# Performance work log

Hardware: AMD Instinct MI355X
Metric: run time of the kernel (lower is better)

The kernel has to match this reference:

```python
import jax, jax.numpy as jnp
import numpy as np

B, S, D, H, FF = 4, 1024, 1024, 8, 4096
DK = D // H
EPS = 1e-5


def layernorm(x, g, b):
    m = jnp.mean(x, axis=-1, keepdims=True)
    v = jnp.mean(jnp.square(x - m), axis=-1, keepdims=True)
    return (x - m) * jax.lax.rsqrt(v + EPS) * g + b


def setup_inputs() -> dict:
    key = jax.random.key(0)
    ks = jax.random.split(key, 8)
    w = lambda k, shape: jax.random.normal(k, shape, jnp.float32) * 0.02
    return {
        "x": jax.random.normal(ks[0], (B, S, D), jnp.float32),
        "mask": jnp.ones((B, 1, 1, S), jnp.int32),  # unused in 'infer' mode, kept for fidelity
        "g1": jnp.ones((D,), jnp.float32), "b1": jnp.zeros((D,), jnp.float32),
        "Wq": w(ks[1], (D, D)), "bq": jnp.zeros((D,), jnp.float32),
        "Wk": w(ks[2], (D, D)), "bk": jnp.zeros((D,), jnp.float32),
        "Wv": w(ks[3], (D, H * D)), "bv": jnp.zeros((H * D,), jnp.float32),
        "g2": jnp.ones((D,), jnp.float32), "b2": jnp.zeros((D,), jnp.float32),
        "W1": w(ks[4], (D, FF)), "bw1": jnp.zeros((FF,), jnp.float32),
        "W2": w(ks[5], (FF, D)), "bw2": jnp.zeros((D,), jnp.float32),
    }


def reference(x, mask, g1, b1, Wq, bq, Wk, bk, Wv, bv, g2, b2, W1, bw1, W2, bw2):
    # --- MultiHeadedAttention (mode='infer'; mask is ignored by this path) ---
    xn = layernorm(x, g1, b1)                                   # [B,S,D]
    q = (xn @ Wq + bq).reshape(B, S, H, DK).transpose(0, 2, 1, 3)  # [B,H,S,DK]
    k = (xn @ Wk + bk).reshape(B, S, H, DK).transpose(0, 2, 1, 3)  # [B,H,S,DK]
    v = (xn @ Wv + bv).reshape(B, S, H, D).transpose(0, 2, 1, 3)   # [B,H,S,D]
    scores = jnp.einsum('bhqd,bhkd->bhqk', q, k) / jnp.sqrt(jnp.float32(DK))
    p = jax.nn.softmax(scores, axis=-1)                          # [B,H,S,S]
    ctx = jnp.einsum('bhqk,bhkd->bhqd', p, v)                    # [B,H,S,D]
    # Source does x.view(-1, B, dim, h).sum(heads).view(B, S, dim) on the
    # contiguous [B,H,S,D] tensor: a raw row-major reshape, reproduced exactly.
    attn_out = ctx.reshape(S, B, D, H).sum(axis=-1).reshape(B, S, D)
    # --- residual + SublayerConnection (pre-norm GELU FFN) ---
    x1 = x + attn_out
    xn2 = layernorm(x1, g2, b2)
    ffn = jax.nn.gelu(xn2 @ W1 + bw1, approximate=False) @ W2 + bw2
    return x1 + ffn
```

## Files before the change

### kernel.cpp

```cpp
#include <hip/hip_runtime.h>
#include <hip/hip_bf16.h>
#include <math.h>

typedef __attribute__((ext_vector_type(8))) short   short8;
typedef __attribute__((ext_vector_type(4))) short   short4v;
typedef __attribute__((ext_vector_type(8))) __bf16  bf16x8;
typedef __attribute__((ext_vector_type(4))) float   f32x4;

typedef const __attribute__((address_space(1))) void cgv_t;
typedef __attribute__((address_space(3))) void lv_t;

__device__ __forceinline__ float bs2f(short s) {
  unsigned int u = ((unsigned int)(unsigned short)s) << 16;
  return __builtin_bit_cast(float, u);
}
__device__ __forceinline__ short f2bs(float f) {
  __hip_bfloat16 h = __float2bfloat16(f);
  return __builtin_bit_cast(short, h);
}
__device__ __forceinline__ void glds16(const short* g, short* l) {
  __builtin_amdgcn_global_load_lds((cgv_t*)g, (lv_t*)l, 16, 0, 0);
}


__global__ __launch_bounds__(256) void transpose_k(const float* __restrict__ in,
                                                   short* __restrict__ out,
                                                   int R, int C) {
  __shared__ __align__(16) short T[64 * 72];
  const int r0 = blockIdx.y * 64, c0 = blockIdx.x * 64;
  const int t = threadIdx.x;
  {
    const int rr = t >> 4;
    const int cc = (t & 15) << 2;
#pragma unroll
    for (int h = 0; h < 4; h++) {
      const int row = rr + h * 16;
      f32x4 v = *(const f32x4*)(in + (long)(r0 + row) * C + c0 + cc);
#pragma unroll
      for (int e = 0; e < 4; e++) T[row * 72 + cc + e] = f2bs(v[e]);
    }
  }
  __syncthreads();
  {
    const int cr = t >> 3;
    const int rs = (t & 7) << 3;
#pragma unroll
    for (int h = 0; h < 2; h++) {
      const int c = cr + h * 32;
      short8 v;
#pragma unroll
      for (int e = 0; e < 8; e++) v[e] = T[(rs + e) * 72 + c];
      *(short8*)(out + (long)(c0 + c) * R + r0 + rs) = v;
    }
  }
}

__global__ __launch_bounds__(256) void tr16_k(const short* __restrict__ in,
                                              short* __restrict__ out) {
  __shared__ __align__(16) short T[64 * 72];
  const int c0 = blockIdx.x * 64;
  const int r0 = blockIdx.y * 64;
  const int t = threadIdx.x;
  {
    const int row = t >> 2, cs = (t & 3) << 4;
    short8 v0 = *(const short8*)(in + (long)(r0 + row) * 1024 + c0 + cs);
    short8 v1 = *(const short8*)(in + (long)(r0 + row) * 1024 + c0 + cs + 8);
    *(short8*)&T[row * 72 + cs] = v0;
    *(short8*)&T[row * 72 + cs + 8] = v1;
  }
  __syncthreads();
  const int bb = r0 >> 10, s0 = r0 & 1023;
  const int cr = t >> 3, rs = (t & 7) << 3;
#pragma unroll
  for (int half = 0; half < 2; half++) {
    const int c = cr + half * 32;
    const int gcol = c0 + c;
    const int head = gcol >> 7, g = gcol & 127;
    short8 v;
#pragma unroll
    for (int e = 0; e < 8; e++) v[e] = T[(rs + e) * 72 + c];
    *(short8*)(out + ((long)(bb * 8 + head)) * 131072 + (long)g * 1024 + s0 + rs) = v;
  }
}

__global__ __launch_bounds__(256) void wv8_k(const float* __restrict__ Wv,
                                             short* __restrict__ out) {
  __shared__ __align__(16) short T[64 * 72];
  const int r0 = blockIdx.x * 64, k0 = blockIdx.y * 64;
  const int t = threadIdx.x;
  const int wave = t >> 6, lane = t & 63;
  const int r = r0 + lane;
#pragma unroll 4
  for (int i = 0; i < 16; i++) {
    const int k = k0 + wave * 16 + i;
    const float* src = Wv + (long)k * 8192 + 8 * r;
    f32x4 a = *(const f32x4*)src;
    f32x4 b = *(const f32x4*)(src + 4);
    float s = (a[0] + a[1] + a[2] + a[3]) + (b[0] + b[1] + b[2] + b[3]);
    T[lane * 72 + wave * 16 + i] = f2bs(s);
  }
  __syncthreads();
  const int rr = t >> 3, kc = (t & 7) << 3;
#pragma unroll
  for (int half = 0; half < 2; half++) {
    const int rl = rr + half * 32;
    *(short8*)(out + (long)(r0 + rl) * 1024 + k0 + kc) = *(const short8*)&T[rl * 72 + kc];
  }
}

__global__ __launch_bounds__(256) void bv8_k(const float* __restrict__ bv,
                                             float* __restrict__ out) {
  const int r = blockIdx.x * 256 + threadIdx.x;
  f32x4 a = *(const f32x4*)(bv + 8 * r);
  f32x4 b = *(const f32x4*)(bv + 8 * r + 4);
  out[r] = (a[0] + a[1] + a[2] + a[3]) + (b[0] + b[1] + b[2] + b[3]);
}

__global__ __launch_bounds__(256) void ln_k(const float* __restrict__ in,
                                            const float* __restrict__ g,
                                            const float* __restrict__ b,
                                            short* __restrict__ out) {
  const int t = threadIdx.x;
  const long base = (long)blockIdx.x * 1024 + t * 4;
  f32x4 f = *(const f32x4*)(in + base);
  float v[4] = {f[0], f[1], f[2], f[3]};
  float s1 = v[0] + v[1] + v[2] + v[3];
  float s2 = v[0]*v[0] + v[1]*v[1] + v[2]*v[2] + v[3]*v[3];
#pragma unroll
  for (int off = 32; off; off >>= 1) {
    s1 += __shfl_xor(s1, off);
    s2 += __shfl_xor(s2, off);
  }
  __shared__ float rs[4], rq[4];
  if ((t & 63) == 0) { rs[t >> 6] = s1; rq[t >> 6] = s2; }
  __syncthreads();
  s1 = rs[0] + rs[1] + rs[2] + rs[3];
  s2 = rq[0] + rq[1] + rq[2] + rq[3];
  const float mean = s1 * (1.0f / 1024.0f);
  const float var  = s2 * (1.0f / 1024.0f) - mean * mean;
  const float rstd = rsqrtf(var + 1e-5f);
  f32x4 gv = *(const f32x4*)(g + t * 4);
  f32x4 bv = *(const f32x4*)(b + t * 4);
  short4v o;
#pragma unroll
  for (int i = 0; i < 4; i++)
    o[i] = f2bs((v[i] - mean) * rstd * gv[i] + bv[i]);
  *(short4v*)(out + base) = o;
}

__global__ __launch_bounds__(256) void reduce4_k(const float* __restrict__ p,
                                                 const float* __restrict__ x1,
                                                 const float* __restrict__ bias,
                                                 float* __restrict__ out) {
  const int t = threadIdx.x;
  const long base = (long)blockIdx.x * 1024 + t * 4;
  f32x4 a = *(const f32x4*)(p + base);
  f32x4 b = *(const f32x4*)(p + 4194304 + base);
  f32x4 c = *(const f32x4*)(p + 8388608 + base);
  f32x4 d = *(const f32x4*)(p + 12582912 + base);
  f32x4 e = *(const f32x4*)(x1 + base);
  f32x4 g = *(const f32x4*)(bias + t * 4);
  *(f32x4*)(out + base) = a + b + c + d + e + g;
}

__global__ __launch_bounds__(256, 2) void flash_k(
    const short* __restrict__ Qg_, const short* __restrict__ Kg_,
    const short* __restrict__ V8T, const float* __restrict__ xg,
    float* __restrict__ x1) {
  __shared__ __align__(16) short smem[40960];
  short* Qs = smem;
  short* Ks = smem + 8192;
  short* Vs = smem + 24576;

  const int t = threadIdx.x;
  const int wave = t >> 6, lane = t & 63;
  const int llo = lane & 15, lhi = lane >> 4;
  const int q0 = blockIdx.x * 64;
  const int bh = blockIdx.y, b = bh >> 3, h = bh & 7;
  const float SC = 0.0883883476483184f;

  const short* Qg = Qg_ + ((long)(b * 1024 + q0)) * 1024 + h * 128;
  const short* Kg = Kg_ + ((long)b * 1024) * 1024 + h * 128;
  const short* Vg = V8T + (long)bh * 131072;

  const int srow = t >> 2, schunk = (t & 3) << 3;
  const int wbase = wave * 512;
  const int arow = (wave * 16 + llo) * 32 + lhi * 8;

#pragma unroll
  for (int kk = 0; kk < 4; kk++)
    glds16(Qg + (long)srow * 1024 + kk * 32 + schunk, Qs + kk * 2048 + wbase);

  f32x4 o[8];
  float mR[4], lR[4];
#pragma unroll
  for (int i = 0; i < 8; i++) o[i] = f32x4{0.f, 0.f, 0.f, 0.f};
#pragma unroll
  for (int r = 0; r < 4; r++) { mR[r] = -1e30f; lR[r] = 0.f; }

  for (int it = 0; it < 8; it++) {
    const int kt0 = it * 128;
#pragma unroll
    for (int kk = 0; kk < 4; kk++) {
      glds16(Kg + (long)(kt0 + srow) * 1024 + kk * 32 + schunk,
             Ks + kk * 4096 + wbase);
      glds16(Kg + (long)(kt0 + 64 + srow) * 1024 + kk * 32 + schunk,
             Ks + kk * 4096 + 2048 + wbase);
      glds16(Vg + (long)srow * 1024 + kt0 + kk * 32 + schunk,
             Vs + kk * 4096 + wbase);
      glds16(Vg + (long)(64 + srow) * 1024 + kt0 + kk * 32 + schunk,
             Vs + kk * 4096 + 2048 + wbase);
    }
    __syncthreads();

    f32x4 s[8];
#pragma unroll
    for (int i = 0; i < 8; i++) s[i] = f32x4{0.f, 0.f, 0.f, 0.f};
#pragma unroll
    for (int kk = 0; kk < 4; kk++) {
      bf16x8 aq = *(const bf16x8*)(Qs + kk * 2048 + arow);
#pragma unroll
      for (int ct = 0; ct < 8; ct++) {
        bf16x8 bk = *(const bf16x8*)(Ks + kk * 4096 + (ct * 16 + llo) * 32 + lhi * 8);
        s[ct] = __builtin_amdgcn_mfma_f32_16x16x32_bf16(aq, bk, s[ct], 0, 0, 0);
      }
    }
#pragma unroll
    for (int ct = 0; ct < 8; ct++)
#pragma unroll
      for (int r = 0; r < 4; r++) s[ct][r] *= SC;
    float alpha[4];
#pragma unroll
    for (int r = 0; r < 4; r++) {
      float mt = s[0][r];
#pragma unroll
      for (int ct = 1; ct < 8; ct++) mt = fmaxf(mt, s[ct][r]);
      mt = fmaxf(mt, __shfl_xor(mt, 1));
      mt = fmaxf(mt, __shfl_xor(mt, 2));
      mt = fmaxf(mt, __shfl_xor(mt, 4));
      mt = fmaxf(mt, __shfl_xor(mt, 8));
      const float mn = fmaxf(mR[r], mt);
      alpha[r] = expf(mR[r] - mn);
      mR[r] = mn;
    }
#pragma unroll
    for (int ct = 0; ct < 8; ct++)
#pragma unroll
      for (int r = 0; r < 4; r++) s[ct][r] = expf(s[ct][r] - mR[r]);
#pragma unroll
    for (int ct = 0; ct < 8; ct++)
#pragma unroll
      for (int r = 0; r < 4; r++) o[ct][r] *= alpha[r];
#pragma unroll
    for (int r = 0; r < 4; r++) {
      float ls = s[0][r];
#pragma unroll
      for (int ct = 1; ct < 8; ct++) ls += s[ct][r];
      ls += __shfl_xor(ls, 1);
      ls += __shfl_xor(ls, 2);
      ls += __shfl_xor(ls, 4);
      ls += __shfl_xor(ls, 8);
      lR[r] = lR[r] * alpha[r] + ls;
    }
    __syncthreads();

#pragma unroll
    for (int ct = 0; ct < 8; ct++) {
      const int base = (ct >> 1) * 4096 + ((ct & 1) << 4) + llo;
#pragma unroll
      for (int r = 0; r < 4; r++)
        Ks[base + (wave * 16 + lhi * 4 + r) * 32] = f2bs(s[ct][r]);
    }
    __syncthreads();

#pragma unroll
    for (int kk = 0; kk < 4; kk++) {
      bf16x8 ap = *(const bf16x8*)(Ks + kk * 4096 + arow);
#pragma unroll
      for (int ct = 0; ct < 8; ct++) {
        bf16x8 bv = *(const bf16x8*)(Vs + kk * 4096 + (ct * 16 + llo) * 32 + lhi * 8);
        o[ct] = __builtin_amdgcn_mfma_f32_16x16x32_bf16(ap, bv, o[ct], 0, 0, 0);
      }
    }
    __syncthreads();
  }

  float inv[4];
#pragma unroll
  for (int r = 0; r < 4; r++) inv[r] = 1.0f / lR[r];
#pragma unroll
  for (int ct = 0; ct < 8; ct++) {
#pragma unroll
    for (int r = 0; r < 4; r++) {
      const int row = q0 + wave * 16 + lhi * 4 + r;
      const long idx = ((long)(b * 8 + h) * 1024 + row) * 128 + ct * 16 + llo;
      x1[idx] = xg[idx] + o[ct][r] * inv[r];
    }
  }
}

enum { E_GELU = 0, E_QKV = 1, E_PART = 2 };

#define MF16(va, vb, vc) __builtin_amdgcn_mfma_f32_16x16x32_bf16(va, vb, vc, 0, 0, 0)
#define VMW(n) asm volatile("s_waitcnt vmcnt(" #n ")" ::: "memory")
#define NOPS ((void)0)

#define STAGE_A(BUF, KH, KB) do {                                          \
    glds16(Ag + (KB), smem + ((BUF) * 2 + (KH)) * 8192 + wofs);            \
    glds16(Ag2 + (KB), smem + ((BUF) * 2 + (KH)) * 8192 + 4096 + wofs);    \
  } while (0)
#define STAGE_B(BUF, KH, KB) do {                                          \
    glds16(Bg + (KB), smem + 32768 + ((BUF) * 2 + (KH)) * 8192 + wofs);    \
    glds16(Bg2 + (KB), smem + 32768 + ((BUF) * 2 + (KH)) * 8192 + 4096 + wofs); \
  } while (0)

#define PHASE(RH, KH, BUF, LOADB, STAGE_STMT, WAIT_STMT)                   \
  {                                                                        \
    const short* Ar_ = smem + ((BUF) * 2 + (KH)) * 8192 + aoff + (RH) * 2048; \
    bf16x8 a0 = *(const bf16x8*)(Ar_);                                     \
    bf16x8 a1 = *(const bf16x8*)(Ar_ + 512);                               \
    bf16x8 a2 = *(const bf16x8*)(Ar_ + 1024);                              \
    bf16x8 a3 = *(const bf16x8*)(Ar_ + 1536);                              \
    if (LOADB) {                                                           \
      const short* Br_ = smem + 32768 + ((BUF) * 2 + (KH)) * 8192 + boff;  \
      vb0 = *(const bf16x8*)(Br_);                                         \
      vb1 = *(const bf16x8*)(Br_ + 512);                                   \
      vb2 = *(const bf16x8*)(Br_ + 1024);                                  \
      vb3 = *(const bf16x8*)(Br_ + 1536);                                  \
    }                                                                      \
    STAGE_STMT;                                                            \
    __builtin_amdgcn_sched_barrier(0);                                     \
    __builtin_amdgcn_s_barrier();                                          \
    asm volatile("s_waitcnt lgkmcnt(0)" ::: "memory");                     \
    __builtin_amdgcn_sched_barrier(0);                                     \
    __builtin_amdgcn_s_setprio(1);                                         \
    acc[(RH) * 4 + 0][0] = MF16(a0, vb0, acc[(RH) * 4 + 0][0]);            \
    acc[(RH) * 4 + 0][1] = MF16(a0, vb1, acc[(RH) * 4 + 0][1]);            \
    acc[(RH) * 4 + 0][2] = MF16(a0, vb2, acc[(RH) * 4 + 0][2]);            \
    acc[(RH) * 4 + 0][3] = MF16(a0, vb3, acc[(RH) * 4 + 0][3]);            \
    acc[(RH) * 4 + 1][0] = MF16(a1, vb0, acc[(RH) * 4 + 1][0]);            \
    acc[(RH) * 4 + 1][1] = MF16(a1, vb1, acc[(RH) * 4 + 1][1]);            \
    acc[(RH) * 4 + 1][2] = MF16(a1, vb2, acc[(RH) * 4 + 1][2]);            \
    acc[(RH) * 4 + 1][3] = MF16(a1, vb3, acc[(RH) * 4 + 1][3]);            \
    acc[(RH) * 4 + 2][0] = MF16(a2, vb0, acc[(RH) * 4 + 2][0]);            \
    acc[(RH) * 4 + 2][1] = MF16(a2, vb1, acc[(RH) * 4 + 2][1]);            \
    acc[(RH) * 4 + 2][2] = MF16(a2, vb2, acc[(RH) * 4 + 2][2]);            \
    acc[(RH) * 4 + 2][3] = MF16(a2, vb3, acc[(RH) * 4 + 2][3]);            \
    acc[(RH) * 4 + 3][0] = MF16(a3, vb0, acc[(RH) * 4 + 3][0]);            \
    acc[(RH) * 4 + 3][1] = MF16(a3, vb1, acc[(RH) * 4 + 3][1]);            \
    acc[(RH) * 4 + 3][2] = MF16(a3, vb2, acc[(RH) * 4 + 3][2]);            \
    acc[(RH) * 4 + 3][3] = MF16(a3, vb3, acc[(RH) * 4 + 3][3]);            \
    __builtin_amdgcn_s_setprio(0);                                         \
    WAIT_STMT;                                                             \
    __builtin_amdgcn_sched_barrier(0);                                     \
    __builtin_amdgcn_s_barrier();                                          \
  }

#define TILE8(T, BUF)                                                        \
  PHASE(0, 0, BUF, 1, STAGE_A(1 - (BUF), 1, ((T) + 1) * 64 + 32), NOPS);     \
  PHASE(1, 0, BUF, 0, STAGE_B(1 - (BUF), 1, ((T) + 1) * 64 + 32), VMW(8));   \
  PHASE(0, 1, BUF, 1, STAGE_A(BUF, 0, ((T) + 2) * 64), NOPS);                \
  PHASE(1, 1, BUF, 0, STAGE_B(BUF, 0, ((T) + 2) * 64), VMW(8))

template <int EPI>
__global__ __launch_bounds__(512, 2) void gemm256(
    const short* __restrict__ A, int lda, long azk,
    const short* __restrict__ Bt, int ldb, long bzk,
    const float* __restrict__ bias, long biasl,
    void* __restrict__ outp, long czl, int ldc,
    void* __restrict__ aux, int K) {
  __shared__ __align__(16) short smem[65536];

  const int t = threadIdx.x;
  const int wave = t >> 6, lane = t & 63;
  const int llo = lane & 15, lhi = lane >> 4;
  const int wm = wave >> 2, wn = wave & 3;

  int lin = blockIdx.x + gridDim.x * (blockIdx.y + gridDim.y * blockIdx.z);
  const int nwg = gridDim.x * gridDim.y * gridDim.z;
  lin = (lin & 7) * (nwg >> 3) + (lin >> 3);
  const int bx = lin % gridDim.x;
  const int rem = lin / gridDim.x;
  const int by = rem % gridDim.y;
  const int z = rem / gridDim.y;

  const int bm0 = by * 256, bn0 = bx * 256;
  A += (long)z * azk;
  Bt += (long)z * bzk;

  const int srow = t >> 2;
  const int sgc = (((t & 3) ^ ((t >> 3) & 3)) << 3);
  const short* Ag  = A  + (long)(bm0 + srow) * lda + sgc;
  const short* Ag2 = A  + (long)(bm0 + 128 + srow) * lda + sgc;
  const short* Bg  = Bt + (long)(bn0 + srow) * ldb + sgc;
  const short* Bg2 = Bt + (long)(bn0 + 128 + srow) * ldb + sgc;
  const int wofs = wave * 512;

  const int swz = ((lhi ^ ((llo >> 1) & 3)) << 3);
  const int aoff = (wm * 128 + llo) * 32 + swz;
  const int boff = (wn * 64 + llo) * 32 + swz;

  f32x4 acc[8][4];
#pragma unroll
  for (int i = 0; i < 8; i++)
#pragma unroll
    for (int j = 0; j < 4; j++) acc[i][j] = f32x4{0.f, 0.f, 0.f, 0.f};
  bf16x8 vb0, vb1, vb2, vb3;

  const int NT = K >> 6;

  STAGE_A(0, 0, 0);  STAGE_B(0, 0, 0);
  STAGE_A(0, 1, 32); STAGE_B(0, 1, 32);
  STAGE_A(1, 0, 64); STAGE_B(1, 0, 64);
  VMW(8);
  __builtin_amdgcn_s_barrier();

  for (int tt = 0; tt < NT - 2; tt += 2) {
    TILE8(tt, 0);
    TILE8(tt + 1, 1);
  }
  PHASE(0, 0, 0, 1, STAGE_A(1, 1, (NT - 1) * 64 + 32), NOPS);
  PHASE(1, 0, 0, 0, STAGE_B(1, 1, (NT - 1) * 64 + 32), VMW(8));
  PHASE(0, 1, 0, 1, NOPS, NOPS);
  PHASE(1, 1, 0, 0, NOPS, VMW(4));
  PHASE(0, 0, 1, 1, NOPS, NOPS);
  PHASE(1, 0, 1, 0, NOPS, VMW(0));
  PHASE(0, 1, 1, 1, NOPS, NOPS);
  PHASE(1, 1, 1, 0, NOPS, NOPS);

  if (EPI == E_PART) {
    float* P = (float*)outp + (long)z * czl;
#pragma unroll
    for (int ct = 0; ct < 4; ct++) {
      const int col = bn0 + wn * 64 + ct * 16 + llo;
#pragma unroll
      for (int rt = 0; rt < 8; rt++) {
#pragma unroll
        for (int r = 0; r < 4; r++) {
          const int row = bm0 + wm * 128 + rt * 16 + lhi * 4 + r;
          P[(long)row * ldc + col] = acc[rt][ct][r];
        }
      }
    }
  } else {
    short* C = (short*)outp + (long)z * czl;
    if (EPI == E_QKV && z == 2) C = (short*)aux;
    short* slab = smem + wave * 4864;
    float bv4[4];
#pragma unroll
    for (int ct = 0; ct < 4; ct++)
      bv4[ct] = bias[z * biasl + bn0 + wn * 64 + ct * 16 + llo];
    const int rl0 = lane >> 3, cb8 = (lane & 7) << 3;
    const short* srd = slab + rl0 * 76 + cb8;
    short* Cw = C + (long)(bm0 + wm * 128 + rl0) * ldc + bn0 + wn * 64 + cb8;
#pragma unroll
    for (int p = 0; p < 2; p++) {
#pragma unroll
      for (int rt4 = 0; rt4 < 4; rt4++) {
#pragma unroll
        for (int ct = 0; ct < 4; ct++) {
#pragma unroll
          for (int r = 0; r < 4; r++) {
            float v = acc[p * 4 + rt4][ct][r] + bv4[ct];
            if (EPI == E_GELU)
              v = 0.5f * v * (1.0f + erff(v * 0.70710678118654752f));
            slab[(rt4 * 16 + lhi * 4 + r) * 76 + ct * 16 + llo] = f2bs(v);
          }
        }
      }
#pragma unroll
      for (int j = 0; j < 8; j++) {
        short8 v = *(const short8*)(srd + j * 8 * 76);
        *(short8*)(Cw + ((long)p * 64 + j * 8) * ldc) = v;
      }
    }
  }
}

extern "C" void kernel_launch(void* const* d_in, const int* in_sizes, int n_in,
                              void* d_out, int out_size, void* d_ws, size_t ws_size,
                              hipStream_t stream) {
  const float* x   = (const float*)d_in[0];
  const float* g1  = (const float*)d_in[2];
  const float* b1  = (const float*)d_in[3];
  const float* Wq  = (const float*)d_in[4];
  const float* bq  = (const float*)d_in[5];
  const float* Wk  = (const float*)d_in[6];
  const float* bk  = (const float*)d_in[7];
  const float* Wv  = (const float*)d_in[8];
  const float* bv  = (const float*)d_in[9];
  const float* g2  = (const float*)d_in[10];
  const float* b2  = (const float*)d_in[11];
  const float* W1  = (const float*)d_in[12];
  const float* bw1 = (const float*)d_in[13];
  const float* W2  = (const float*)d_in[14];
  const float* bw2 = (const float*)d_in[15];

  char* ws = (char*)d_ws;
  const long MB = 1024 * 1024;
  float* bQKV  = (float*)(ws);
  float* x1    = (float*)(ws + 1 * MB);
  short* wqT   = (short*)(ws + 17 * MB);
  short* wkT   = (short*)(ws + 19 * MB);
  short* wv8T  = (short*)(ws + 21 * MB);
  short* xn    = (short*)(ws + 23 * MB);
  short* Q     = (short*)(ws + 31 * MB);
  short* Kb    = (short*)(ws + 39 * MB);
  short* V8T   = (short*)(ws + 47 * MB);
  short* V8tmp = (short*)(ws + 55 * MB);
  short* xn2  = (short*)(ws + 17 * MB);
  short* Hb   = (short*)(ws + 25 * MB);
  short* w1T  = (short*)(ws + 57 * MB);
  short* w2T  = (short*)(ws + 65 * MB);
  float* part = (float*)(ws + 73 * MB);

  hipMemcpyAsync(bQKV, bq, 4096, hipMemcpyDeviceToDevice, stream);
  hipMemcpyAsync(bQKV + 1024, bk, 4096, hipMemcpyDeviceToDevice, stream);
  bv8_k<<<4, 256, 0, stream>>>(bv, bQKV + 2048);

  transpose_k<<<dim3(16, 16), 256, 0, stream>>>(Wq, wqT, 1024, 1024);
  transpose_k<<<dim3(16, 16), 256, 0, stream>>>(Wk, wkT, 1024, 1024);
  wv8_k<<<dim3(16, 16), 256, 0, stream>>>(Wv, wv8T);

  ln_k<<<4096, 256, 0, stream>>>(x, g1, b1, xn);

  gemm256<E_QKV><<<dim3(4, 16, 3), 512, 0, stream>>>(
      xn, 1024, 0, wqT, 1024, 1048576, bQKV, 1024,
      Q, 4194304, 1024, V8tmp, 1024);

  tr16_k<<<dim3(16, 64), 256, 0, stream>>>(V8tmp, V8T);

  flash_k<<<dim3(16, 32), 256, 0, stream>>>(Q, Kb, V8T, x, x1);

  transpose_k<<<dim3(64, 16), 256, 0, stream>>>(W1, w1T, 1024, 4096);
  transpose_k<<<dim3(16, 64), 256, 0, stream>>>(W2, w2T, 4096, 1024);

  ln_k<<<4096, 256, 0, stream>>>(x1, g2, b2, xn2);

  gemm256<E_GELU><<<dim3(16, 16, 1), 512, 0, stream>>>(
      xn2, 1024, 0, w1T, 1024, 0, bw1, 0,
      Hb, 0, 4096, nullptr, 1024);

  gemm256<E_PART><<<dim3(4, 16, 4), 512, 0, stream>>>(
      Hb, 4096, 1024, w2T, 4096, 1024, nullptr, 0,
      part, 4194304, 1024, nullptr, 1024);

  reduce4_k<<<4096, 256, 0, stream>>>(part, x1, bw2, (float*)d_out);
}
```

Baseline: 370.2 us.

## Swizzle flash-attention LDS tiles and fold softmax scale into Q projection

Applies an XOR swizzle to the 16-byte chunk index of the Q, K, V and P tiles in LDS, in both the global-to-LDS loads and the MFMA operand reads, to cut LDS bank conflicts. It also removes the per-element score scaling by multiplying Q by scale*log2(e) in the QKV GEMM epilogue. The softmax then uses the hardware exp2 instruction instead of expf. This relies on the swizzle matching across all writers and readers, and rounding the prescaled Q to bf16 slightly changes the numerics.

```diff
diff --git a/kernel.cpp b/kernel.cpp
--- a/kernel.cpp
+++ b/kernel.cpp
@@ -177,19 +177,20 @@
   const int llo = lane & 15, lhi = lane >> 4;
   const int q0 = blockIdx.x * 64;
   const int bh = blockIdx.y, b = bh >> 3, h = bh & 7;
-  const float SC = 0.0883883476483184f;
 
   const short* Qg = Qg_ + ((long)(b * 1024 + q0)) * 1024 + h * 128;
   const short* Kg = Kg_ + ((long)b * 1024) * 1024 + h * 128;
   const short* Vg = V8T + (long)bh * 131072;
 
-  const int srow = t >> 2, schunk = (t & 3) << 3;
+  const int srow = t >> 2;
+  const int sgc = (((t & 3) ^ ((t >> 3) & 3)) << 3);
   const int wbase = wave * 512;
-  const int arow = (wave * 16 + llo) * 32 + lhi * 8;
+  const int swzo = ((lhi ^ ((llo >> 1) & 3)) << 3);
+  const int arow = (wave * 16 + llo) * 32 + swzo;
 
 #pragma unroll
   for (int kk = 0; kk < 4; kk++)
-    glds16(Qg + (long)srow * 1024 + kk * 32 + schunk, Qs + kk * 2048 + wbase);
+    glds16(Qg + (long)srow * 1024 + kk * 32 + sgc, Qs + kk * 2048 + wbase);
 
   f32x4 o[8];
   float mR[4], lR[4];
@@ -202,13 +203,13 @@
     const int kt0 = it * 128;
 #pragma unroll
     for (int kk = 0; kk < 4; kk++) {
-      glds16(Kg + (long)(kt0 + srow) * 1024 + kk * 32 + schunk,
+      glds16(Kg + (long)(kt0 + srow) * 1024 + kk * 32 + sgc,
              Ks + kk * 4096 + wbase);
-      glds16(Kg + (long)(kt0 + 64 + srow) * 1024 + kk * 32 + schunk,
+      glds16(Kg + (long)(kt0 + 64 + srow) * 1024 + kk * 32 + sgc,
              Ks + kk * 4096 + 2048 + wbase);
-      glds16(Vg + (long)srow * 1024 + kt0 + kk * 32 + schunk,
+      glds16(Vg + (long)srow * 1024 + kt0 + kk * 32 + sgc,
              Vs + kk * 4096 + wbase);
-      glds16(Vg + (long)(64 + srow) * 1024 + kt0 + kk * 32 + schunk,
+      glds16(Vg + (long)(64 + srow) * 1024 + kt0 + kk * 32 + sgc,
              Vs + kk * 4096 + 2048 + wbase);
     }
     __syncthreads();
@@ -221,14 +222,10 @@
       bf16x8 aq = *(const bf16x8*)(Qs + kk * 2048 + arow);
 #pragma unroll
       for (int ct = 0; ct < 8; ct++) {
-        bf16x8 bk = *(const bf16x8*)(Ks + kk * 4096 + (ct * 16 + llo) * 32 + lhi * 8);
+        bf16x8 bk = *(const bf16x8*)(Ks + kk * 4096 + (ct * 16 + llo) * 32 + swzo);
         s[ct] = __builtin_amdgcn_mfma_f32_16x16x32_bf16(aq, bk, s[ct], 0, 0, 0);
       }
     }
-#pragma unroll
-    for (int ct = 0; ct < 8; ct++)
-#pragma unroll
-      for (int r = 0; r < 4; r++) s[ct][r] *= SC;
     float alpha[4];
 #pragma unroll
     for (int r = 0; r < 4; r++) {
@@ -240,13 +237,14 @@
       mt = fmaxf(mt, __shfl_xor(mt, 4));
       mt = fmaxf(mt, __shfl_xor(mt, 8));
       const float mn = fmaxf(mR[r], mt);
-      alpha[r] = expf(mR[r] - mn);
+      alpha[r] = __builtin_amdgcn_exp2f(mR[r] - mn);
       mR[r] = mn;
     }
 #pragma unroll
     for (int ct = 0; ct < 8; ct++)
 #pragma unroll
-      for (int r = 0; r < 4; r++) s[ct][r] = expf(s[ct][r] - mR[r]);
+      for (int r = 0; r < 4; r++)
+        s[ct][r] = __builtin_amdgcn_exp2f(s[ct][r] - mR[r]);
 #pragma unroll
     for (int ct = 0; ct < 8; ct++)
 #pragma unroll
@@ -266,10 +264,14 @@
 
 #pragma unroll
     for (int ct = 0; ct < 8; ct++) {
-      const int base = (ct >> 1) * 4096 + ((ct & 1) << 4) + llo;
-#pragma unroll
-      for (int r = 0; r < 4; r++)
-        Ks[base + (wave * 16 + lhi * 4 + r) * 32] = f2bs(s[ct][r]);
+      const int chunk = ((ct & 1) << 1) | (llo >> 3);
+      const int cl = llo & 7;
+#pragma unroll
+      for (int r = 0; r < 4; r++) {
+        const int row = wave * 16 + lhi * 4 + r;
+        const int xr = ((lhi << 1) | (r >> 1)) & 3;
+        Ks[(ct >> 1) * 4096 + row * 32 + (((chunk ^ xr) << 3) | cl)] = f2bs(s[ct][r]);
+      }
     }
     __syncthreads();
 
@@ -278,7 +280,7 @@
       bf16x8 ap = *(const bf16x8*)(Ks + kk * 4096 + arow);
 #pragma unroll
       for (int ct = 0; ct < 8; ct++) {
-        bf16x8 bv = *(const bf16x8*)(Vs + kk * 4096 + (ct * 16 + llo) * 32 + lhi * 8);
+        bf16x8 bv = *(const bf16x8*)(Vs + kk * 4096 + (ct * 16 + llo) * 32 + swzo);
         o[ct] = __builtin_amdgcn_mfma_f32_16x16x32_bf16(ap, bv, o[ct], 0, 0, 0);
       }
     }
@@ -464,6 +466,8 @@
             float v = acc[p * 4 + rt4][ct][r] + bv4[ct];
             if (EPI == E_GELU)
               v = 0.5f * v * (1.0f + erff(v * 0.70710678118654752f));
+            if (EPI == E_QKV && z == 0)
+              v *= 0.12751744476582f;
             slab[(rt4 * 16 + lhi * 4 + r) * 76 + ct * 16 + llo] = f2bs(v);
           }
         }
```

Result: faster. 359.5 us (-2.9%).
